# Optimization experiments

Measured on AMD Instinct MI355X. Metric: run time of the kernel, lower is better.

## Reference

```python
import jax, jax.numpy as jnp
import numpy as np

N = 50000
E = 1_600_000
F_IN = 128
HID = 64
OUT = 2
NEG_SLOPE = 0.2  # PyG GATConv default


def setup_inputs() -> dict:
    key = jax.random.key(0)
    ks = jax.random.split(key, 10)
    x = jax.random.normal(ks[0], (N, F_IN), jnp.float32)
    edge_index = jax.random.randint(ks[1], (2, E), 0, N, dtype=jnp.int32)
    # glorot-ish scaled params
    W1 = jax.random.normal(ks[2], (F_IN, HID), jnp.float32) / np.sqrt(F_IN)
    a1_src = jax.random.normal(ks[3], (HID,), jnp.float32) / np.sqrt(HID)
    a1_dst = jax.random.normal(ks[4], (HID,), jnp.float32) / np.sqrt(HID)
    b1 = jnp.zeros((HID,), jnp.float32)
    W2 = jax.random.normal(ks[5], (HID, OUT), jnp.float32) / np.sqrt(HID)
    a2_src = jax.random.normal(ks[6], (OUT,), jnp.float32) / np.sqrt(OUT)
    a2_dst = jax.random.normal(ks[7], (OUT,), jnp.float32) / np.sqrt(OUT)
    b2 = jnp.zeros((OUT,), jnp.float32)
    return {"x": x, "edge_index": edge_index, "W1": W1, "a1_src": a1_src,
            "a1_dst": a1_dst, "b1": b1, "W2": W2, "a2_src": a2_src,
            "a2_dst": a2_dst, "b2": b2}


def gat_layer(x, edge_index, W, a_src, a_dst, b):
    n = x.shape[0]
    loop = jnp.arange(n, dtype=edge_index.dtype)
    src = jnp.concatenate([edge_index[0], loop])  # [E+N] message sources j
    dst = jnp.concatenate([edge_index[1], loop])  # [E+N] message targets i
    h = x @ W                                     # [N, out]
    alpha_s = h @ a_src                           # [N]
    alpha_d = h @ a_dst                           # [N]
    e = jax.nn.leaky_relu(alpha_s[src] + alpha_d[dst], NEG_SLOPE)  # [E+N]
    # segment softmax over edges sharing the same destination node
    emax = jax.ops.segment_max(e, dst, num_segments=n)
    ee = jnp.exp(e - emax[dst])
    denom = jax.ops.segment_sum(ee, dst, num_segments=n)
    alpha = ee / denom[dst]
    out = jax.ops.segment_sum(alpha[:, None] * h[src], dst, num_segments=n)
    return out + b


def reference(x, edge_index, W1, a1_src, a1_dst, b1, W2, a2_src, a2_dst, b2):
    h = gat_layer(x, edge_index, W1, a1_src, a1_dst, b1)
    h = jax.nn.relu(h)
    # dropout(p=0.5) is identity in eval mode
    return gat_layer(h, edge_index, W2, a2_src, a2_dst, b2)
```

## Files before the change

kernel.cpp:

```cpp
#include <hip/hip_runtime.h>
#include <hip/hip_fp16.h>
#include <math.h>


#define NEG 0.2f
#define NEGINF (-1e30f)

#define BPW   128
#define NB    391
#define BLKS  192
#define SCAP  64
#define CAPB  4864

__device__ __forceinline__ float leaky(float v) { return v >= 0.f ? v : NEG * v; }

__global__ __launch_bounds__(256) void k_gemm_bucket(
    const float* __restrict__ x, const float* __restrict__ W1,
    const float* __restrict__ a1s_, const float* __restrict__ a1d_,
    const int* __restrict__ esrc, const int* __restrict__ edst, int N, int E,
    __half* __restrict__ h1h, float* __restrict__ as1, float* __restrict__ ad1,
    int* __restrict__ slabs, int* __restrict__ slabcnt) {
    __shared__ int cnt[NB];
    int t = threadIdx.x;
    if ((int)blockIdx.x < BLKS) {
        int blk = blockIdx.x;
        for (int i = t; i < NB; i += 256) cnt[i] = 0;
        __syncthreads();
        int chunk = (E + BLKS - 1) / BLKS;
        int lo = blk * chunk, hi = min(E, lo + chunk);
        for (int e = lo + t; e < hi; e += 256) {
            int s = esrc[e], d = edst[e];
            int b = d >> 7;
            int pos = atomicAdd(&cnt[b], 1);
            if (pos < SCAP)
                slabs[((size_t)b * BLKS + blk) * SCAP + pos] = s | ((d & 127) << 16);
        }
        __syncthreads();
        for (int i = t; i < NB; i += 256)
            slabcnt[i * BLKS + blk] = min(cnt[i], SCAP);
    } else {
        int gb = blockIdx.x - BLKS;
        int lane = t & 63;
        int wid = __builtin_amdgcn_readfirstlane(t >> 6);
        int r0 = __builtin_amdgcn_readfirstlane(gb * 16 + wid * 4);
        if (r0 >= N) return;
        const float4* x0 = (const float4*)(x + (size_t)r0 * 128);
        const float4* x1 = (const float4*)(x + (size_t)(r0 + 1) * 128);
        const float4* x2 = (const float4*)(x + (size_t)(r0 + 2) * 128);
        const float4* x3 = (const float4*)(x + (size_t)(r0 + 3) * 128);
        float acc0 = 0.f, acc1 = 0.f, acc2 = 0.f, acc3 = 0.f;
#pragma unroll 8
        for (int k4 = 0; k4 < 32; k4++) {
            int kb = k4 * 4;
            float w0 = W1[(kb + 0) * 64 + lane];
            float w1 = W1[(kb + 1) * 64 + lane];
            float w2 = W1[(kb + 2) * 64 + lane];
            float w3 = W1[(kb + 3) * 64 + lane];
            float4 a = x0[k4], bb = x1[k4], c = x2[k4], d = x3[k4];
            acc0 = fmaf(a.x, w0, fmaf(a.y, w1, fmaf(a.z, w2, fmaf(a.w, w3, acc0))));
            acc1 = fmaf(bb.x, w0, fmaf(bb.y, w1, fmaf(bb.z, w2, fmaf(bb.w, w3, acc1))));
            acc2 = fmaf(c.x, w0, fmaf(c.y, w1, fmaf(c.z, w2, fmaf(c.w, w3, acc2))));
            acc3 = fmaf(d.x, w0, fmaf(d.y, w1, fmaf(d.z, w2, fmaf(d.w, w3, acc3))));
        }
        float asv = a1s_[lane], adv = a1d_[lane];
        float accs[4] = {acc0, acc1, acc2, acc3};
#pragma unroll
        for (int r = 0; r < 4; r++) {
            int row = r0 + r;
            if (row < N) h1h[(size_t)row * 64 + lane] = __float2half_rn(accs[r]);
            float ts = accs[r] * asv, td = accs[r] * adv;
            for (int m = 32; m > 0; m >>= 1) {
                ts += __shfl_xor(ts, m, 64);
                td += __shfl_xor(td, m, 64);
            }
            if (lane == 0 && row < N) { as1[row] = ts; ad1[row] = td; }
        }
    }
}

__global__ __launch_bounds__(256) void k_sortb(
    const int* __restrict__ slabs, const int* __restrict__ slabcnt, int N,
    int* __restrict__ ssrc32, int* __restrict__ nodebase,
    int* __restrict__ nodedeg) {
    __shared__ int cstage[CAPB];
    __shared__ unsigned short outs[CAPB];
    __shared__ int ccnt[BLKS];
    __shared__ int coff[BLKS];
    __shared__ int hist[BPW], pexcl[BPW], cur[BPW];
    __shared__ int ctotS, btotS;
    int b = blockIdx.x, t = threadIdx.x;

    for (int i = t; i < BLKS; i += 256) ccnt[i] = slabcnt[b * BLKS + i];
    for (int i = t; i < BPW; i += 256) hist[i] = 0;
    __syncthreads();

    if (t < 64) {
        int carry = 0;
        for (int c0 = 0; c0 < BLKS; c0 += 64) {
            int v = ccnt[c0 + t];
            int incl = v;
            for (int off = 1; off < 64; off <<= 1) {
                int u = __shfl_up(incl, off, 64);
                if (t >= off) incl += u;
            }
            coff[c0 + t] = carry + incl - v;
            carry += __shfl(incl, 63, 64);
        }
        if (t == 0) ctotS = carry;
    }
    __syncthreads();
    int ctot = min(ctotS, CAPB);

    for (int c = t; c < BLKS; c += 256) {
        int cn = ccnt[c], off = coff[c];
        const int* cell = slabs + ((size_t)b * BLKS + c) * SCAP;
        for (int j = 0; j < cn; j++) {
            int p = off + j;
            if (p < CAPB) cstage[p] = cell[j];
        }
    }
    __syncthreads();

    for (int i = t; i < ctot; i += 256) atomicAdd(&hist[cstage[i] >> 16], 1);
    __syncthreads();

    if (t < 64) {
        int h0 = hist[2 * t], h1v = hist[2 * t + 1];
        int p0 = (h0 + 3) & ~3, p1 = (h1v + 3) & ~3;
        int ps = p0 + p1, incl = ps;
        for (int off = 1; off < 64; off <<= 1) {
            int u = __shfl_up(incl, off, 64);
            if (t >= off) incl += u;
        }
        int ex = incl - ps;
        pexcl[2 * t] = ex;          cur[2 * t] = ex;
        pexcl[2 * t + 1] = ex + p0; cur[2 * t + 1] = ex + p0;
        if (t == 63) btotS = incl;
    }
    __syncthreads();

    for (int i = t; i < ctot; i += 256) {
        int en = cstage[i];
        int p = atomicAdd(&cur[en >> 16], 1);
        if (p < CAPB) outs[p] = (unsigned short)(en & 0xFFFF);
    }
    __syncthreads();

    int v0 = b * BPW;
    for (int i = t; i < BPW; i += 256) {
        int h = hist[i], ph = (h + 3) & ~3;
        for (int j = h; j < ph; j++) {
            int pos = pexcl[i] + j;
            if (pos < CAPB) outs[pos] = (unsigned short)(v0 + i);
        }
    }
    __syncthreads();

    int btot = min(btotS, CAPB);
    int* dst = ssrc32 + (size_t)b * CAPB;
    for (int i = t; i < btot; i += 256) dst[i] = (int)outs[i];

    for (int i = t; i < BPW; i += 256) {
        int v = v0 + i;
        if (v < N) { nodebase[v] = b * CAPB + pexcl[i]; nodedeg[v] = hist[i]; }
    }
}

__global__ __launch_bounds__(256) void k_agg1f(
    const __half* __restrict__ h1h, const float* __restrict__ as1,
    const float* __restrict__ ad1, const int* __restrict__ nodebase,
    const int* __restrict__ nodedeg, const int* __restrict__ ssrc32,
    const float* __restrict__ b1, const float* __restrict__ W2,
    const float* __restrict__ a2s, const float* __restrict__ a2d, int N,
    float4* __restrict__ node4) {
    __shared__ __align__(16) float pw[4][128];
    int lane = threadIdx.x & 63;
    int wid = __builtin_amdgcn_readfirstlane(threadIdx.x >> 6);
    int i = blockIdx.x * 4 + wid;
    if (i >= N) return;
    float ad_i = ad1[i];
    int base = nodebase[i], deg = nodedeg[i];

    float e0 = NEGINF, e1 = NEGINF;
    if (lane < deg)      e0 = leaky(as1[ssrc32[base + lane]] + ad_i);
    if (lane + 64 < deg) e1 = leaky(as1[ssrc32[base + lane + 64]] + ad_i);
    float ml = fmaxf(e0, e1), sl = 0.f;
    for (int t = base + lane + 128; t < base + deg; t += 64) {
        float e = leaky(as1[ssrc32[t]] + ad_i);
        float mN = fmaxf(ml, e);
        sl = sl * __expf(ml - mN) + __expf(e - mN);
        ml = mN;
    }
    sl += __expf(e0 - ml) + __expf(e1 - ml);
    for (int off = 32; off > 0; off >>= 1) {
        float m2 = __shfl_xor(ml, off, 64);
        float s2 = __shfl_xor(sl, off, 64);
        float mN = fmaxf(ml, m2);
        sl = sl * __expf(ml - mN) + s2 * __expf(m2 - mN);
        ml = mN;
    }
    float e_self = leaky(as1[i] + ad_i);
    float m = fmaxf(ml, e_self);
    float s = sl * __expf(ml - m) + __expf(e_self - m);
    float inv_s = 1.f / s;

    pw[wid][lane]      = (lane < deg)      ? __expf(e0 - m) * inv_s : 0.f;
    pw[wid][lane + 64] = (lane + 64 < deg) ? __expf(e1 - m) * inv_s : 0.f;

    int nq = (min(deg, 128) + 3) >> 2;
    const int4* sq = (const int4*)(ssrc32 + base);
    float acc = __expf(e_self - m) * inv_s * __half2float(h1h[(size_t)i * 64 + lane]);
#pragma unroll 2
    for (int q = 0; q < nq; ++q) {
        int4 s4 = sq[q];
        float4 p4 = *(const float4*)&pw[wid][q * 4];
        float g0 = __half2float(h1h[(size_t)s4.x * 64 + lane]);
        float g1 = __half2float(h1h[(size_t)s4.y * 64 + lane]);
        float g2 = __half2float(h1h[(size_t)s4.z * 64 + lane]);
        float g3 = __half2float(h1h[(size_t)s4.w * 64 + lane]);
        acc = fmaf(p4.x, g0, acc);
        acc = fmaf(p4.y, g1, acc);
        acc = fmaf(p4.z, g2, acc);
        acc = fmaf(p4.w, g3, acc);
    }
    for (int t = base + 128; t < base + deg; ++t) {
        int sv = ssrc32[t];
        float p = __expf(leaky(as1[sv] + ad_i) - m) * inv_s;
        acc = fmaf(p, __half2float(h1h[(size_t)sv * 64 + lane]), acc);
    }

    float hr = fmaxf(acc + b1[lane], 0.f);
    float2 w2 = ((const float2*)W2)[lane];
    float t0 = hr * w2.x, t1 = hr * w2.y;
    for (int mm = 32; mm > 0; mm >>= 1) {
        t0 += __shfl_xor(t0, mm, 64);
        t1 += __shfl_xor(t1, mm, 64);
    }
    if (lane == 0) {
        float s0 = t0 * a2s[0] + t1 * a2s[1];
        float d0 = t0 * a2d[0] + t1 * a2d[1];
        node4[i] = make_float4(t0, t1, s0, d0);
    }
}

__global__ __launch_bounds__(256) void k_agg2(
    const float4* __restrict__ node4, const int* __restrict__ nodebase,
    const int* __restrict__ nodedeg, const int* __restrict__ ssrc32,
    const float* __restrict__ b2, int N, float2* __restrict__ out) {
    int lane = threadIdx.x & 63, wid = threadIdx.x >> 6;
    int i = blockIdx.x * 4 + wid;
    if (i >= N) return;
    float4 ni = node4[i];
    float adi = ni.w;
    int base = nodebase[i], end = base + nodedeg[i];
    float ml = NEGINF, sl = 0.f, A0 = 0.f, A1 = 0.f;
    for (int t = base + lane; t < end; t += 64) {
        float4 nd = node4[ssrc32[t]];
        float e = leaky(nd.z + adi);
        float mN = fmaxf(ml, e);
        float c1 = __expf(ml - mN), p = __expf(e - mN);
        sl = fmaf(sl, c1, p);
        A0 = fmaf(A0, c1, p * nd.x);
        A1 = fmaf(A1, c1, p * nd.y);
        ml = mN;
    }
    for (int off = 32; off > 0; off >>= 1) {
        float m2 = __shfl_xor(ml, off, 64);
        float s2 = __shfl_xor(sl, off, 64);
        float a02 = __shfl_xor(A0, off, 64);
        float a12 = __shfl_xor(A1, off, 64);
        float mN = fmaxf(ml, m2);
        float c1 = __expf(ml - mN), c2 = __expf(m2 - mN);
        sl = sl * c1 + s2 * c2;
        A0 = A0 * c1 + a02 * c2;
        A1 = A1 * c1 + a12 * c2;
        ml = mN;
    }
    float e_self = leaky(ni.z + adi);
    float mN = fmaxf(ml, e_self);
    float c1 = __expf(ml - mN), c2 = __expf(e_self - mN);
    float s = sl * c1 + c2;
    float a0 = A0 * c1 + c2 * ni.x;
    float a1 = A1 * c1 + c2 * ni.y;
    if (lane == 0) out[i] = make_float2(a0 / s + b2[0], a1 / s + b2[1]);
}

extern "C" void kernel_launch(void* const* d_in, const int* in_sizes, int n_in,
                              void* d_out, int out_size, void* d_ws, size_t ws_size,
                              hipStream_t stream) {
    const float* x   = (const float*)d_in[0];
    const int*   ei  = (const int*)d_in[1];
    const float* W1  = (const float*)d_in[2];
    const float* a1s = (const float*)d_in[3];
    const float* a1d = (const float*)d_in[4];
    const float* b1  = (const float*)d_in[5];
    const float* W2  = (const float*)d_in[6];
    const float* a2s = (const float*)d_in[7];
    const float* a2d = (const float*)d_in[8];
    const float* b2  = (const float*)d_in[9];

    int N = in_sizes[0] / 128;
    int E = in_sizes[1] / 2;
    const int* esrc = ei;
    const int* edst = ei + E;

    __half* h1h   = (__half*)d_ws;
    float*  as1   = (float*)(h1h + (size_t)N * 64);
    float*  ad1   = as1 + N;
    float*  pad0  = ad1 + N;
    float4* node4 = (float4*)(pad0 + N);
    int* slabs    = (int*)(node4 + N);
    int* slabcnt  = slabs + (size_t)NB * BLKS * SCAP;
    int* ssrc32   = slabcnt + (size_t)NB * BLKS;
    int* nodebase = ssrc32 + (size_t)NB * CAPB;
    int* nodedeg  = nodebase + N;

    int nbG = (N + 15) / 16;
    k_gemm_bucket<<<BLKS + nbG, 256, 0, stream>>>(x, W1, a1s, a1d, esrc, edst,
                                                  N, E, h1h, as1, ad1, slabs, slabcnt);
    k_sortb<<<NB, 256, 0, stream>>>(slabs, slabcnt, N, ssrc32, nodebase, nodedeg);
    k_agg1f<<<(N + 3) / 4, 256, 0, stream>>>(h1h, as1, ad1, nodebase, nodedeg,
                                             ssrc32, b1, W2, a2s, a2d, N, node4);
    k_agg2<<<(N + 3) / 4, 256, 0, stream>>>(node4, nodebase, nodedeg, ssrc32, b2,
                                            N, (float2*)d_out);
}
```

Baseline: 189.5 us.

## Split fused bucket/GEMM kernel and retile GEMM with LDS-staged rows

```diff
diff --git a/kernel.cpp b/kernel.cpp
--- a/kernel.cpp
+++ b/kernel.cpp
@@ -14,67 +14,90 @@
 
 __device__ __forceinline__ float leaky(float v) { return v >= 0.f ? v : NEG * v; }
 
-__global__ __launch_bounds__(256) void k_gemm_bucket(
-    const float* __restrict__ x, const float* __restrict__ W1,
-    const float* __restrict__ a1s_, const float* __restrict__ a1d_,
-    const int* __restrict__ esrc, const int* __restrict__ edst, int N, int E,
-    __half* __restrict__ h1h, float* __restrict__ as1, float* __restrict__ ad1,
+__global__ __launch_bounds__(256) void k_bucket(
+    const int* __restrict__ esrc, const int* __restrict__ edst, int E,
     int* __restrict__ slabs, int* __restrict__ slabcnt) {
     __shared__ int cnt[NB];
+    int t = threadIdx.x, blk = blockIdx.x;
+    for (int i = t; i < NB; i += 256) cnt[i] = 0;
+    __syncthreads();
+    int chunk = (E + BLKS - 1) / BLKS;
+    int lo = blk * chunk, hi = min(E, lo + chunk);
+    for (int e = lo + t; e < hi; e += 256) {
+        int s = esrc[e], d = edst[e];
+        int b = d >> 7;
+        int pos = atomicAdd(&cnt[b], 1);
+        if (pos < SCAP)
+            slabs[((size_t)b * BLKS + blk) * SCAP + pos] = s | ((d & 127) << 16);
+    }
+    __syncthreads();
+    for (int i = t; i < NB; i += 256)
+        slabcnt[i * BLKS + blk] = min(cnt[i], SCAP);
+}
+
+__global__ __launch_bounds__(256) void k_gemm(
+    const float* __restrict__ x, const float* __restrict__ W1,
+    const float* __restrict__ a1s_, const float* __restrict__ a1d_, int N,
+    __half* __restrict__ h1h, float* __restrict__ as1, float* __restrict__ ad1) {
+    __shared__ float xs[64][129];
+    __shared__ float red[2][4][64];
     int t = threadIdx.x;
-    if ((int)blockIdx.x < BLKS) {
-        int blk = blockIdx.x;
-        for (int i = t; i < NB; i += 256) cnt[i] = 0;
-        __syncthreads();
-        int chunk = (E + BLKS - 1) / BLKS;
-        int lo = blk * chunk, hi = min(E, lo + chunk);
-        for (int e = lo + t; e < hi; e += 256) {
-            int s = esrc[e], d = edst[e];
-            int b = d >> 7;
-            int pos = atomicAdd(&cnt[b], 1);
-            if (pos < SCAP)
-                slabs[((size_t)b * BLKS + blk) * SCAP + pos] = s | ((d & 127) << 16);
-        }
-        __syncthreads();
-        for (int i = t; i < NB; i += 256)
-            slabcnt[i * BLKS + blk] = min(cnt[i], SCAP);
-    } else {
-        int gb = blockIdx.x - BLKS;
-        int lane = t & 63;
-        int wid = __builtin_amdgcn_readfirstlane(t >> 6);
-        int r0 = __builtin_amdgcn_readfirstlane(gb * 16 + wid * 4);
-        if (r0 >= N) return;
-        const float4* x0 = (const float4*)(x + (size_t)r0 * 128);
-        const float4* x1 = (const float4*)(x + (size_t)(r0 + 1) * 128);
-        const float4* x2 = (const float4*)(x + (size_t)(r0 + 2) * 128);
-        const float4* x3 = (const float4*)(x + (size_t)(r0 + 3) * 128);
-        float acc0 = 0.f, acc1 = 0.f, acc2 = 0.f, acc3 = 0.f;
-#pragma unroll 8
-        for (int k4 = 0; k4 < 32; k4++) {
-            int kb = k4 * 4;
-            float w0 = W1[(kb + 0) * 64 + lane];
-            float w1 = W1[(kb + 1) * 64 + lane];
-            float w2 = W1[(kb + 2) * 64 + lane];
-            float w3 = W1[(kb + 3) * 64 + lane];
-            float4 a = x0[k4], bb = x1[k4], c = x2[k4], d = x3[k4];
-            acc0 = fmaf(a.x, w0, fmaf(a.y, w1, fmaf(a.z, w2, fmaf(a.w, w3, acc0))));
-            acc1 = fmaf(bb.x, w0, fmaf(bb.y, w1, fmaf(bb.z, w2, fmaf(bb.w, w3, acc1))));
-            acc2 = fmaf(c.x, w0, fmaf(c.y, w1, fmaf(c.z, w2, fmaf(c.w, w3, acc2))));
-            acc3 = fmaf(d.x, w0, fmaf(d.y, w1, fmaf(d.z, w2, fmaf(d.w, w3, acc3))));
-        }
-        float asv = a1s_[lane], adv = a1d_[lane];
-        float accs[4] = {acc0, acc1, acc2, acc3};
-#pragma unroll
-        for (int r = 0; r < 4; r++) {
-            int row = r0 + r;
-            if (row < N) h1h[(size_t)row * 64 + lane] = __float2half_rn(accs[r]);
-            float ts = accs[r] * asv, td = accs[r] * adv;
-            for (int m = 32; m > 0; m >>= 1) {
-                ts += __shfl_xor(ts, m, 64);
-                td += __shfl_xor(td, m, 64);
-            }
-            if (lane == 0 && row < N) { as1[row] = ts; ad1[row] = td; }
-        }
+    int r0 = blockIdx.x * 64;
+    {
+        const float4* xg = (const float4*)x;
+        for (int j = 0; j < 8; j++) {
+            int idx = t + j * 256;
+            int row = idx >> 5, c4 = idx & 31;
+            float4 v = make_float4(0.f, 0.f, 0.f, 0.f);
+            if (r0 + row < N) v = xg[(size_t)(r0 + row) * 32 + c4];
+            *(float4*)&xs[row][c4 * 4] = v;
+        }
+    }
+    __syncthreads();
+    int lane = t & 63;
+    int wid = __builtin_amdgcn_readfirstlane(t >> 6);
+    const float* Wp = W1 + 16 * wid;
+    float acc[16];
+#pragma unroll
+    for (int j = 0; j < 16; j++) acc[j] = 0.f;
+#pragma unroll 4
+    for (int k4 = 0; k4 < 32; k4++) {
+        float4 xv = *(const float4*)&xs[lane][k4 * 4];
+#pragma unroll
+        for (int kk = 0; kk < 4; kk++) {
+            const float* wrow = Wp + (k4 * 4 + kk) * 64;
+            float xk = (kk == 0) ? xv.x : (kk == 1) ? xv.y : (kk == 2) ? xv.z : xv.w;
+#pragma unroll
+            for (int j = 0; j < 16; j++) acc[j] = fmaf(xk, wrow[j], acc[j]);
+        }
+    }
+    int row = r0 + lane;
+    float ps = 0.f, pd = 0.f;
+#pragma unroll
+    for (int j = 0; j < 16; j++) {
+        ps = fmaf(acc[j], a1s_[16 * wid + j], ps);
+        pd = fmaf(acc[j], a1d_[16 * wid + j], pd);
+    }
+    red[0][wid][lane] = ps;
+    red[1][wid][lane] = pd;
+    if (row < N) {
+        unsigned int pk[8];
+#pragma unroll
+        for (int j = 0; j < 8; j++) {
+            __half2 h2 = __floats2half2_rn(acc[2 * j], acc[2 * j + 1]);
+            pk[j] = *(unsigned int*)&h2;
+        }
+        __half* dst = h1h + (size_t)row * 64 + 16 * wid;
+        ((int4*)dst)[0] = make_int4(pk[0], pk[1], pk[2], pk[3]);
+        ((int4*)dst)[1] = make_int4(pk[4], pk[5], pk[6], pk[7]);
+    }
+    __syncthreads();
+    if (t < 64) {
+        int r = r0 + t;
+        if (r < N) as1[r] = red[0][0][t] + red[0][1][t] + red[0][2][t] + red[0][3][t];
+    } else if (t < 128) {
+        int t2 = t - 64, r = r0 + t2;
+        if (r < N) ad1[r] = red[1][0][t2] + red[1][1][t2] + red[1][2][t2] + red[1][3][t2];
     }
 }
 
@@ -315,9 +338,8 @@
     int* nodebase = ssrc32 + (size_t)NB * CAPB;
     int* nodedeg  = nodebase + N;
 
-    int nbG = (N + 15) / 16;
-    k_gemm_bucket<<<BLKS + nbG, 256, 0, stream>>>(x, W1, a1s, a1d, esrc, edst,
-                                                  N, E, h1h, as1, ad1, slabs, slabcnt);
+    k_bucket<<<BLKS, 256, 0, stream>>>(esrc, edst, E, slabs, slabcnt);
+    k_gemm<<<(N + 63) / 64, 256, 0, stream>>>(x, W1, a1s, a1d, N, h1h, as1, ad1);
     k_sortb<<<NB, 256, 0, stream>>>(slabs, slabcnt, N, ssrc32, nodebase, nodedeg);
     k_agg1f<<<(N + 3) / 4, 256, 0, stream>>>(h1h, as1, ad1, nodebase, nodedeg,
                                              ssrc32, b1, W2, a2s, a2d, N, node4);
```

Result: slower. 201.9 us (+6.6%).
